# Optimization experiments

Hardware: AMD Instinct MI355X
Metric: run time of the kernel (lower is better)

## Reference

```python
import jax, jax.numpy as jnp
import numpy as np

NEG_SLOPE = 0.2
EPS = 1e-16  # PyG softmax denominator epsilon


def gatv2_layer(x, src, dst, W_l, W_r, att, bias, num_nodes, heads, out_dim, concat):
    # x: [N, F_in]; src/dst: [E] (self-loops already included)
    x_l = (x @ W_l).reshape(num_nodes, heads, out_dim)  # source transform
    x_r = (x @ W_r).reshape(num_nodes, heads, out_dim)  # target transform
    # GATv2 scoring: a^T LeakyReLU(x_l[j] + x_r[i])
    e = jax.nn.leaky_relu(x_l[src] + x_r[dst], NEG_SLOPE)       # [E, H, D]
    logits = jnp.einsum('ehd,hd->eh', e, att)                    # [E, H]
    # segment softmax over incoming edges of each target node
    m = jax.ops.segment_max(logits, dst, num_segments=num_nodes)  # [N, H]
    ex = jnp.exp(logits - m[dst])                                 # [E, H]
    denom = jax.ops.segment_sum(ex, dst, num_segments=num_nodes)  # [N, H]
    alpha = ex / (denom[dst] + EPS)                               # [E, H]
    msg = x_l[src] * alpha[:, :, None]                            # [E, H, D]
    out = jax.ops.segment_sum(msg, dst, num_segments=num_nodes)   # [N, H, D]
    if concat:
        out = out.reshape(num_nodes, heads * out_dim)
    else:
        out = out.mean(axis=1)
    return out + bias


def setup_inputs() -> dict:
    key = jax.random.key(0)
    ks = jax.random.split(key, 10)
    N, E, F_in, H, D, F_out = 50000, 400000, 256, 4, 128, 64

    def glorot(k, shape, fan):
        return jax.random.normal(k, shape, dtype=jnp.float32) * (1.0 / np.sqrt(fan))

    return {
        'x': jax.random.normal(ks[0], (N, F_in), dtype=jnp.float32),
        'edge_index': jax.random.randint(ks[1], (2, E), 0, N, dtype=jnp.int64),
        'W_l1': glorot(ks[2], (F_in, H * D), F_in),
        'W_r1': glorot(ks[3], (F_in, H * D), F_in),
        'att1': glorot(ks[4], (H, D), D),
        'b1': jnp.zeros((H * D,), dtype=jnp.float32),
        'W_l2': glorot(ks[5], (H * D, F_out), H * D),
        'W_r2': glorot(ks[6], (H * D, F_out), H * D),
        'att2': glorot(ks[7], (1, F_out), F_out),
        'b2': jnp.zeros((F_out,), dtype=jnp.float32),
    }


def reference(x, edge_index, W_l1, W_r1, att1, b1, W_l2, W_r2, att2, b2):
    N = x.shape[0]
    # add self-loops (PyG GATv2Conv default add_self_loops=True)
    loops = jnp.arange(N, dtype=edge_index.dtype)
    src = jnp.concatenate([edge_index[0], loops])
    dst = jnp.concatenate([edge_index[1], loops])
    # dropout(p=0.6) is identity in eval mode
    h = gatv2_layer(x, src, dst, W_l1, W_r1, att1, b1, N, heads=4, out_dim=128, concat=True)
    h = jax.nn.elu(h)
    out = gatv2_layer(h, src, dst, W_l2, W_r2, att2, b2, N, heads=1, out_dim=64, concat=False)
    return out
```

## Files before the change

### kernel.cpp

```cpp
#include <hip/hip_runtime.h>
#include <hip/hip_bf16.h>
#include <math.h>


#define NEG_SLOPE 0.2f
#define LOG2E 1.4426950408889634f

typedef _Float16 half8 __attribute__((ext_vector_type(8)));
typedef _Float16 h2 __attribute__((ext_vector_type(2)));
typedef float f32x4 __attribute__((ext_vector_type(4)));

#if __has_builtin(__builtin_amdgcn_global_load_lds)
#define HAS_GLL 1
__device__ __forceinline__ void gll16(const _Float16* g, _Float16* l) {
    __builtin_amdgcn_global_load_lds(
        (const __attribute__((address_space(1))) unsigned int*)g,
        (__attribute__((address_space(3))) unsigned int*)l, 16, 0, 0);
}
#endif

__device__ __forceinline__ float dot2acc(h2 a, h2 b, float c) {
#if __has_builtin(__builtin_amdgcn_fdot2)
    return __builtin_amdgcn_fdot2(a, b, c, false);
#else
    return fmaf((float)a[1], (float)b[1], fmaf((float)a[0], (float)b[0], c));
#endif
}

__device__ __forceinline__ float fast_exp2(float p) {
#if __has_builtin(__builtin_amdgcn_exp2f)
    return __builtin_amdgcn_exp2f(p);
#else
    return exp2f(p);
#endif
}


__global__ __launch_bounds__(256) void k_castx_count(const float* __restrict__ x, _Float16* __restrict__ xh,
                                                     int n8, const int* __restrict__ ei,
                                                     int* __restrict__ counts, int E, int Etot, int gEtot) {
    int b = blockIdx.x;
    if (b < gEtot) {
        int i = b * 256 + threadIdx.x;
        if (i < Etot) {
            int dst = (i < E) ? ei[E + i] : (i - E);
            atomicAdd(&counts[dst], 1);
        }
    } else {
        int i = (b - gEtot) * 256 + threadIdx.x;
        if (i < n8) {
            const float4* p = (const float4*)(x + i * 8);
            float4 a = p[0], c = p[1];
            half8 v;
            v[0] = (_Float16)a.x; v[1] = (_Float16)a.y; v[2] = (_Float16)a.z; v[3] = (_Float16)a.w;
            v[4] = (_Float16)c.x; v[5] = (_Float16)c.y; v[6] = (_Float16)c.z; v[7] = (_Float16)c.w;
            *(half8*)(xh + i * 8) = v;
        }
    }
}


__global__ __launch_bounds__(1024) void k_castw_scana(const int* __restrict__ counts, int* __restrict__ offs,
                                                      int* __restrict__ partial, int n, int nsb,
                                                      const float* __restrict__ Wl1, const float* __restrict__ Wr1,
                                                      const float* __restrict__ Wl2, const float* __restrict__ Wr2,
                                                      _Float16* __restrict__ W1T, _Float16* __restrict__ W2T) {
    __shared__ int buf[1024];
    int b = blockIdx.x, t = threadIdx.x;
    if (b < nsb) {
        int i = b * 1024 + t;
        int v = (i < n) ? counts[i] : 0;
        buf[t] = v;
        __syncthreads();
        #pragma unroll
        for (int off = 1; off < 1024; off <<= 1) {
            int add = (t >= off) ? buf[t - off] : 0;
            __syncthreads();
            buf[t] += add;
            __syncthreads();
        }
        if (i < n) offs[i + 1] = buf[t];
        if (t == 1023) partial[b] = buf[1023];
    } else {
        int i = (b - nsb) * 1024 + t;
        const int T1 = 1024 * 256;
        const int T2 = 128 * 512;
        if (i < T1) {
            int nn = i >> 8, k = i & 255;
            float v = (nn < 512) ? Wl1[k * 512 + nn] : Wr1[k * 512 + (nn - 512)];
            W1T[i] = (_Float16)v;
        } else if (i < T1 + T2) {
            int j = i - T1;
            int nn = j >> 9, k = j & 511;
            float v = (nn < 64) ? Wl2[k * 64 + nn] : Wr2[k * 64 + (nn - 64)];
            W2T[j] = (_Float16)v;
        }
    }
}


__global__ __launch_bounds__(256) void k_scanbc(int* __restrict__ offs, int* __restrict__ cursor,
                                                const int* __restrict__ partial, int n, int nsb) {
    __shared__ int s[256];
    int t = threadIdx.x;
    int v = (t < nsb) ? partial[t] : 0;
    s[t] = v;
    __syncthreads();
    #pragma unroll
    for (int off = 1; off < 256; off <<= 1) {
        int add = (t >= off) ? s[t - off] : 0;
        __syncthreads();
        s[t] += add;
        __syncthreads();
    }
    int excl = s[t] - v;
    s[t] = excl;
    __syncthreads();
    int i = blockIdx.x * 256 + t;
    if (i == 0) { offs[0] = 0; cursor[0] = 0; }
    if (i < n) {
        int w = offs[i + 1] + s[i >> 10];
        offs[i + 1] = w;
        cursor[i + 1] = w;
    }
}


__device__ __forceinline__ void gemm_body(const _Float16* __restrict__ A,
                                          const _Float16* __restrict__ Bt,
                                          _Float16* __restrict__ C,
                                          int M, int N, int K, int ntiles, int blk,
                                          _Float16* As, _Float16* Bs) {
    int tid = threadIdx.x;
    int lane = tid & 63;
    int wave = tid >> 6;
    int wm = wave >> 1, wn = wave & 1;
    int l15 = lane & 15, q = lane >> 4;

    int ntile = blk % ntiles;
    int mtile = blk / ntiles;
    int tileM = mtile * 128;
    int tileN = ntile * 128;

    int srow = lane >> 2;
    int schunk = (lane & 3) ^ ((lane >> 3) & 3);
    const _Float16* gA0 = A + (long)(tileM + wave * 32 + srow) * K + schunk * 8;
    const _Float16* gA1 = gA0 + (long)16 * K;
    const _Float16* gB0 = Bt + (long)(tileN + wave * 32 + srow) * K + schunk * 8;
    const _Float16* gB1 = gB0 + (long)16 * K;
    _Float16* lA0 = As + wave * 1024;
    _Float16* lA1 = lA0 + 512;
    _Float16* lB0 = Bs + wave * 1024;
    _Float16* lB1 = lB0 + 512;

    int aswz = (q ^ ((l15 >> 1) & 3)) * 8;

    f32x4 acc[4][4];
    #pragma unroll
    for (int i = 0; i < 4; ++i)
        #pragma unroll
        for (int j = 0; j < 4; ++j)
            acc[i][j] = (f32x4)(0.f);

    for (int k0 = 0; k0 < K; k0 += 32) {
#ifdef HAS_GLL
        gll16(gA0 + k0, lA0);
        gll16(gA1 + k0, lA1);
        gll16(gB0 + k0, lB0);
        gll16(gB1 + k0, lB1);
#else
        half8 va0 = *(const half8*)(gA0 + k0);
        half8 va1 = *(const half8*)(gA1 + k0);
        half8 vb0 = *(const half8*)(gB0 + k0);
        half8 vb1 = *(const half8*)(gB1 + k0);
        *(half8*)(lA0 + lane * 8) = va0;
        *(half8*)(lA1 + lane * 8) = va1;
        *(half8*)(lB0 + lane * 8) = vb0;
        *(half8*)(lB1 + lane * 8) = vb1;
#endif
        __syncthreads();

        half8 af[4], bf[4];
        #pragma unroll
        for (int i = 0; i < 4; ++i)
            af[i] = *(const half8*)(As + (wm * 64 + i * 16 + l15) * 32 + aswz);
        #pragma unroll
        for (int j = 0; j < 4; ++j)
            bf[j] = *(const half8*)(Bs + (wn * 64 + j * 16 + l15) * 32 + aswz);
        #pragma unroll
        for (int i = 0; i < 4; ++i)
            #pragma unroll
            for (int j = 0; j < 4; ++j)
                acc[i][j] = __builtin_amdgcn_mfma_f32_16x16x32_f16(af[i], bf[j], acc[i][j], 0, 0, 0);
        __syncthreads();
    }

    #pragma unroll
    for (int i = 0; i < 4; ++i) {
        #pragma unroll
        for (int r = 0; r < 4; ++r) {
            int grow = tileM + wm * 64 + i * 16 + q * 4 + r;
            if (grow < M) {
                #pragma unroll
                for (int j = 0; j < 4; ++j) {
                    int gcol = tileN + wn * 64 + j * 16 + l15;
                    C[(long)grow * N + gcol] = (_Float16)acc[i][j][r];
                }
            }
        }
    }
}

__global__ __launch_bounds__(256) void k_gemm1_fill(const _Float16* __restrict__ A,
                                                    const _Float16* __restrict__ Bt,
                                                    _Float16* __restrict__ C,
                                                    int M, int N, int K, int ntiles, int gb,
                                                    const int* __restrict__ ei, int* __restrict__ cursor,
                                                    int* __restrict__ csr_src, int E, int Etot) {
    __shared__ _Float16 As[128 * 32];
    __shared__ _Float16 Bs[128 * 32];
    int b = blockIdx.x;
    if (b < gb) {
        gemm_body(A, Bt, C, M, N, K, ntiles, b, As, Bs);
    } else {
        int i = (b - gb) * 256 + threadIdx.x;
        if (i < Etot) {
            int src, dst;
            if (i < E) { src = ei[i]; dst = ei[E + i]; }
            else       { src = i - E; dst = i - E; }
            int pos = atomicAdd(&cursor[dst], 1);
            csr_src[pos] = src;
        }
    }
}

__global__ __launch_bounds__(256) void k_gemm_f16(const _Float16* __restrict__ A,
                                                  const _Float16* __restrict__ Bt,
                                                  _Float16* __restrict__ C,
                                                  int M, int N, int K, int ntiles) {
    __shared__ _Float16 As[128 * 32];
    __shared__ _Float16 Bs[128 * 32];
    gemm_body(A, Bt, C, M, N, K, ntiles, blockIdx.x, As, Bs);
}


__global__ __launch_bounds__(256) void k_attn1(const _Float16* __restrict__ xlr,
                                               const float* __restrict__ att, const float* __restrict__ b1,
                                               const int* __restrict__ offs, const int* __restrict__ csr_src,
                                               _Float16* __restrict__ hout, int N) {
    int wave = threadIdx.x >> 6;
    int lane = threadIdx.x & 63;
    int node = blockIdx.x * 4 + wave;
    if (node >= N) return;

    int cbase = (lane >> 4) * 128 + (lane & 15) * 8;

    half8 xrv8 = *(const half8*)(xlr + (long)node * 1024 + 512 + cbase);
    float4 atv0 = *(const float4*)(att + cbase);
    float4 atv1 = *(const float4*)(att + cbase + 4);
    h2 xr[4], at[4];
    #pragma unroll
    for (int j = 0; j < 4; ++j) {
        xr[j][0] = xrv8[2 * j]; xr[j][1] = xrv8[2 * j + 1];
    }
    at[0][0] = (_Float16)(atv0.x * LOG2E); at[0][1] = (_Float16)(atv0.y * LOG2E);
    at[1][0] = (_Float16)(atv0.z * LOG2E); at[1][1] = (_Float16)(atv0.w * LOG2E);
    at[2][0] = (_Float16)(atv1.x * LOG2E); at[2][1] = (_Float16)(atv1.y * LOG2E);
    at[3][0] = (_Float16)(atv1.z * LOG2E); at[3][1] = (_Float16)(atv1.w * LOG2E);
    const h2 ns2 = {(_Float16)NEG_SLOPE, (_Float16)NEG_SLOPE};

    float l = 0.f;
    float acc[8] = {};

    int e0 = offs[node], e1 = offs[node + 1];
    int s_next = csr_src[e0];
    int s_next2 = (e0 + 1 < e1) ? csr_src[e0 + 1] : 0;
    half8 xlv = *(const half8*)(xlr + (long)s_next * 1024 + cbase);

    for (int e = e0; e < e1; ++e) {
        half8 cur = xlv;
        int s_pf = s_next2;
        if (e + 2 < e1) s_next2 = csr_src[e + 2];
        if (e + 1 < e1) xlv = *(const half8*)(xlr + (long)s_pf * 1024 + cbase);

        const h2* cp = (const h2*)&cur;
        float p = 0.f;
        #pragma unroll
        for (int j = 0; j < 4; ++j) {
            h2 t = cp[j] + xr[j];
#if __has_builtin(__builtin_elementwise_max)
            t = __builtin_elementwise_max(t, t * ns2);
#else
            h2 tn = t * ns2;
            t[0] = (t[0] > tn[0]) ? t[0] : tn[0];
            t[1] = (t[1] > tn[1]) ? t[1] : tn[1];
#endif
            p = dot2acc(t, at[j], p);
        }
        #pragma unroll
        for (int off = 1; off <= 8; off <<= 1) p += __shfl_xor(p, off, 64);
        float w = fast_exp2(p);
        l += w;
        #pragma unroll
        for (int j = 0; j < 8; ++j) acc[j] = fmaf(w, (float)cur[j], acc[j]);
    }

    float inv = 1.f / (l + 1e-16f);
    float4 b1v0 = *(const float4*)(b1 + cbase);
    float4 b1v1 = *(const float4*)(b1 + cbase + 4);
    float bb[8] = {b1v0.x, b1v0.y, b1v0.z, b1v0.w, b1v1.x, b1v1.y, b1v1.z, b1v1.w};
    half8 ov;
    #pragma unroll
    for (int j = 0; j < 8; ++j) {
        float o = fmaf(acc[j], inv, bb[j]);
        o = (o > 0.f) ? o : (__expf(o) - 1.f);
        ov[j] = (_Float16)o;
    }
    *(half8*)(hout + (long)node * 512 + cbase) = ov;
}


__global__ __launch_bounds__(256) void k_attn2(const _Float16* __restrict__ xlr2,
                                               const float* __restrict__ att, const float* __restrict__ b2,
                                               const int* __restrict__ offs, const int* __restrict__ csr_src,
                                               float* __restrict__ out, int N) {
    int wave = threadIdx.x >> 6;
    int lane = threadIdx.x & 63;
    int node = blockIdx.x * 4 + wave;
    if (node >= N) return;

    int eh = lane >> 5;
    int hl = lane & 31;
    int ch = hl * 2;

    h2 xrh = *(const h2*)(xlr2 + (long)node * 128 + 64 + ch);
    float2 atf = *(const float2*)(att + ch);
    h2 ath; ath[0] = (_Float16)(atf.x * LOG2E); ath[1] = (_Float16)(atf.y * LOG2E);
    const h2 ns2 = {(_Float16)NEG_SLOPE, (_Float16)NEG_SLOPE};

    float l = 0.f, a0 = 0.f, a1 = 0.f;
    int e0 = offs[node], e1 = offs[node + 1];
    int e = e0 + eh;
    h2 cv;
    if (e < e1) {
        int s = csr_src[e];
        cv = *(const h2*)(xlr2 + (long)s * 128 + ch);
    }
    while (e < e1) {
        h2 u = cv;
        int en = e + 2;
        if (en < e1) {
            int s = csr_src[en];
            cv = *(const h2*)(xlr2 + (long)s * 128 + ch);
        }
        h2 t = u + xrh;
#if __has_builtin(__builtin_elementwise_max)
        t = __builtin_elementwise_max(t, t * ns2);
#else
        h2 tn = t * ns2;
        t[0] = (t[0] > tn[0]) ? t[0] : tn[0];
        t[1] = (t[1] > tn[1]) ? t[1] : tn[1];
#endif
        float p = dot2acc(t, ath, 0.f);
        p += __shfl_xor(p, 1, 64);
        p += __shfl_xor(p, 2, 64);
        p += __shfl_xor(p, 4, 64);
        p += __shfl_xor(p, 8, 64);
        p += __shfl_xor(p, 16, 64);
        float w = fast_exp2(p);
        l += w;
        a0 = fmaf(w, (float)u[0], a0);
        a1 = fmaf(w, (float)u[1], a1);
        e = en;
    }
    l += __shfl_xor(l, 32, 64);
    a0 += __shfl_xor(a0, 32, 64);
    a1 += __shfl_xor(a1, 32, 64);
    if (eh == 0) {
        float inv = 1.f / (l + 1e-16f);
        float2 o;
        o.x = fmaf(a0, inv, b2[ch]);
        o.y = fmaf(a1, inv, b2[ch + 1]);
        *(float2*)(out + (long)node * 64 + ch) = o;
    }
}


extern "C" void kernel_launch(void* const* d_in, const int* in_sizes, int n_in,
                              void* d_out, int out_size, void* d_ws, size_t ws_size,
                              hipStream_t stream) {
    const float* x    = (const float*)d_in[0];
    const int*   ei   = (const int*)d_in[1];
    const float* Wl1  = (const float*)d_in[2];
    const float* Wr1  = (const float*)d_in[3];
    const float* att1 = (const float*)d_in[4];
    const float* b1   = (const float*)d_in[5];
    const float* Wl2  = (const float*)d_in[6];
    const float* Wr2  = (const float*)d_in[7];
    const float* att2 = (const float*)d_in[8];
    const float* b2   = (const float*)d_in[9];
    float* out = (float*)d_out;

    const int F_IN = 256;
    int N = in_sizes[0] / F_IN;
    int E = in_sizes[1] / 2;
    int Etot = E + N;
    int nScanBlocks = (N + 1023) / 1024;
    int mtiles = (N + 127) / 128;
    int Mpad = mtiles * 128;

    char* p = (char*)d_ws;
    auto carve = [&](size_t bytes) -> void* {
        void* r = (void*)p;
        p += (bytes + 255) & ~(size_t)255;
        return r;
    };
    _Float16* xh   = (_Float16*)carve((size_t)Mpad * 256 * 2);
    _Float16* W1T  = (_Float16*)carve((size_t)1024 * 256 * 2);
    _Float16* W2T  = (_Float16*)carve((size_t)128 * 512 * 2);
    _Float16* C1   = (_Float16*)carve((size_t)N * 1024 * 2);
    _Float16* h    = (_Float16*)carve((size_t)Mpad * 512 * 2);
    _Float16* C2   = (_Float16*)carve((size_t)N * 128 * 2);
    int* counts  = (int*)carve((size_t)N * 4);
    int* offs    = (int*)carve((size_t)(N + 1) * 4);
    int* cursor  = (int*)carve((size_t)(N + 1) * 4);
    int* partial = (int*)carve((size_t)nScanBlocks * 4);
    int* csr     = (int*)carve((size_t)Etot * 4);

    int gN    = (N + 255) / 256;
    int gEtot = (Etot + 255) / 256;
    int n8    = N * 256 / 8;
    int gCast = (n8 + 255) / 256;

    hipMemsetAsync(counts, 0, (size_t)N * 4, stream);

    k_castx_count<<<gEtot + gCast, 256, 0, stream>>>(x, xh, n8, ei, counts, E, Etot, gEtot);

    {
        int total = 1024 * 256 + 128 * 512;
        int gW = (total + 1023) / 1024;
        k_castw_scana<<<nScanBlocks + gW, 1024, 0, stream>>>(counts, offs, partial, N, nScanBlocks,
                                                             Wl1, Wr1, Wl2, Wr2, W1T, W2T);
    }
    k_scanbc<<<gN, 256, 0, stream>>>(offs, cursor, partial, N, nScanBlocks);

    {
        int gb = mtiles * 8;
        k_gemm1_fill<<<gb + gEtot, 256, 0, stream>>>(xh, W1T, C1, N, 1024, 256, 8, gb,
                                                     ei, cursor, csr, E, Etot);
    }
    k_attn1<<<(N + 3) / 4, 256, 0, stream>>>(C1, att1, b1, offs, csr, h, N);

    k_gemm_f16<<<mtiles, 256, 0, stream>>>(h, W2T, C2, N, 128, 512, 1);
    k_attn2<<<(N + 3) / 4, 256, 0, stream>>>(C2, att2, b2, offs, csr, out, N);
}
```

Measured before the change: 334.1 us.

## Use 512-thread GEMM blocks with 4x2 wave grid and packed FMA in attention

The GEMM kernels move from 256 to 512 threads per 128x128 tile, arranged as a 2x4 wave grid. Each wave now loads one 16-row slice per k-step and computes a 64x32 sub-tile, which cuts accumulator registers per thread and doubles the waves available to hide latency. The attention kernels switch to unsigned shift-based gather addressing and float2 vector FMAs so the compiler can emit packed FMA. The fill path is resized to 512 threads per block to match. The trade-off is less B-fragment reuse per wave and more sync participants per tile.

```diff
diff --git a/kernel.cpp b/kernel.cpp
--- a/kernel.cpp
+++ b/kernel.cpp
@@ -9,6 +9,7 @@
 typedef _Float16 half8 __attribute__((ext_vector_type(8)));
 typedef _Float16 h2 __attribute__((ext_vector_type(2)));
 typedef float f32x4 __attribute__((ext_vector_type(4)));
+typedef float f32x2 __attribute__((ext_vector_type(2)));
 
 #if __has_builtin(__builtin_amdgcn_global_load_lds)
 #define HAS_GLL 1
@@ -134,7 +135,7 @@
     int tid = threadIdx.x;
     int lane = tid & 63;
     int wave = tid >> 6;
-    int wm = wave >> 1, wn = wave & 1;
+    int wm = wave >> 2, wn = wave & 3;
     int l15 = lane & 15, q = lane >> 4;
 
     int ntile = blk % ntiles;
@@ -144,53 +145,43 @@
 
     int srow = lane >> 2;
     int schunk = (lane & 3) ^ ((lane >> 3) & 3);
-    const _Float16* gA0 = A + (long)(tileM + wave * 32 + srow) * K + schunk * 8;
-    const _Float16* gA1 = gA0 + (long)16 * K;
-    const _Float16* gB0 = Bt + (long)(tileN + wave * 32 + srow) * K + schunk * 8;
-    const _Float16* gB1 = gB0 + (long)16 * K;
-    _Float16* lA0 = As + wave * 1024;
-    _Float16* lA1 = lA0 + 512;
-    _Float16* lB0 = Bs + wave * 1024;
-    _Float16* lB1 = lB0 + 512;
+    const _Float16* gA = A + (long)(tileM + wave * 16 + srow) * K + schunk * 8;
+    const _Float16* gB = Bt + (long)(tileN + wave * 16 + srow) * K + schunk * 8;
+    _Float16* lA = As + wave * 512;
+    _Float16* lB = Bs + wave * 512;
 
     int aswz = (q ^ ((l15 >> 1) & 3)) * 8;
 
-    f32x4 acc[4][4];
+    f32x4 acc[4][2];
     #pragma unroll
     for (int i = 0; i < 4; ++i)
         #pragma unroll
-        for (int j = 0; j < 4; ++j)
+        for (int j = 0; j < 2; ++j)
             acc[i][j] = (f32x4)(0.f);
 
     for (int k0 = 0; k0 < K; k0 += 32) {
 #ifdef HAS_GLL
-        gll16(gA0 + k0, lA0);
-        gll16(gA1 + k0, lA1);
-        gll16(gB0 + k0, lB0);
-        gll16(gB1 + k0, lB1);
+        gll16(gA + k0, lA);
+        gll16(gB + k0, lB);
 #else
-        half8 va0 = *(const half8*)(gA0 + k0);
-        half8 va1 = *(const half8*)(gA1 + k0);
-        half8 vb0 = *(const half8*)(gB0 + k0);
-        half8 vb1 = *(const half8*)(gB1 + k0);
-        *(half8*)(lA0 + lane * 8) = va0;
-        *(half8*)(lA1 + lane * 8) = va1;
-        *(half8*)(lB0 + lane * 8) = vb0;
-        *(half8*)(lB1 + lane * 8) = vb1;
+        half8 va = *(const half8*)(gA + k0);
+        half8 vb = *(const half8*)(gB + k0);
+        *(half8*)(lA + lane * 8) = va;
+        *(half8*)(lB + lane * 8) = vb;
 #endif
         __syncthreads();
 
-        half8 af[4], bf[4];
+        half8 af[4], bf[2];
         #pragma unroll
         for (int i = 0; i < 4; ++i)
             af[i] = *(const half8*)(As + (wm * 64 + i * 16 + l15) * 32 + aswz);
         #pragma unroll
-        for (int j = 0; j < 4; ++j)
-            bf[j] = *(const half8*)(Bs + (wn * 64 + j * 16 + l15) * 32 + aswz);
+        for (int j = 0; j < 2; ++j)
+            bf[j] = *(const half8*)(Bs + (wn * 32 + j * 16 + l15) * 32 + aswz);
         #pragma unroll
         for (int i = 0; i < 4; ++i)
             #pragma unroll
-            for (int j = 0; j < 4; ++j)
+            for (int j = 0; j < 2; ++j)
                 acc[i][j] = __builtin_amdgcn_mfma_f32_16x16x32_f16(af[i], bf[j], acc[i][j], 0, 0, 0);
         __syncthreads();
     }
@@ -202,8 +193,8 @@
             int grow = tileM + wm * 64 + i * 16 + q * 4 + r;
             if (grow < M) {
                 #pragma unroll
-                for (int j = 0; j < 4; ++j) {
-                    int gcol = tileN + wn * 64 + j * 16 + l15;
+                for (int j = 0; j < 2; ++j) {
+                    int gcol = tileN + wn * 32 + j * 16 + l15;
                     C[(long)grow * N + gcol] = (_Float16)acc[i][j][r];
                 }
             }
@@ -211,7 +202,7 @@
     }
 }
 
-__global__ __launch_bounds__(256) void k_gemm1_fill(const _Float16* __restrict__ A,
+__global__ __launch_bounds__(512) void k_gemm1_fill(const _Float16* __restrict__ A,
                                                     const _Float16* __restrict__ Bt,
                                                     _Float16* __restrict__ C,
                                                     int M, int N, int K, int ntiles, int gb,
@@ -223,7 +214,7 @@
     if (b < gb) {
         gemm_body(A, Bt, C, M, N, K, ntiles, b, As, Bs);
     } else {
-        int i = (b - gb) * 256 + threadIdx.x;
+        int i = (b - gb) * 512 + threadIdx.x;
         if (i < Etot) {
             int src, dst;
             if (i < E) { src = ei[i]; dst = ei[E + i]; }
@@ -234,7 +225,7 @@
     }
 }
 
-__global__ __launch_bounds__(256) void k_gemm_f16(const _Float16* __restrict__ A,
+__global__ __launch_bounds__(512) void k_gemm_f16(const _Float16* __restrict__ A,
                                                   const _Float16* __restrict__ Bt,
                                                   _Float16* __restrict__ C,
                                                   int M, int N, int K, int ntiles) {
@@ -254,8 +245,9 @@
     if (node >= N) return;
 
     int cbase = (lane >> 4) * 128 + (lane & 15) * 8;
-
-    half8 xrv8 = *(const half8*)(xlr + (long)node * 1024 + 512 + cbase);
+    const _Float16* xlr_l = xlr + cbase;
+
+    half8 xrv8 = *(const half8*)(xlr_l + ((unsigned)node << 10) + 512);
     float4 atv0 = *(const float4*)(att + cbase);
     float4 atv1 = *(const float4*)(att + cbase + 4);
     h2 xr[4], at[4];
@@ -270,18 +262,20 @@
     const h2 ns2 = {(_Float16)NEG_SLOPE, (_Float16)NEG_SLOPE};
 
     float l = 0.f;
-    float acc[8] = {};
+    f32x2 acc[4];
+    #pragma unroll
+    for (int j = 0; j < 4; ++j) acc[j] = (f32x2)(0.f);
 
     int e0 = offs[node], e1 = offs[node + 1];
     int s_next = csr_src[e0];
     int s_next2 = (e0 + 1 < e1) ? csr_src[e0 + 1] : 0;
-    half8 xlv = *(const half8*)(xlr + (long)s_next * 1024 + cbase);
+    half8 xlv = *(const half8*)(xlr_l + ((unsigned)s_next << 10));
 
     for (int e = e0; e < e1; ++e) {
         half8 cur = xlv;
         int s_pf = s_next2;
         if (e + 2 < e1) s_next2 = csr_src[e + 2];
-        if (e + 1 < e1) xlv = *(const half8*)(xlr + (long)s_pf * 1024 + cbase);
+        if (e + 1 < e1) xlv = *(const half8*)(xlr_l + ((unsigned)s_pf << 10));
 
         const h2* cp = (const h2*)&cur;
         float p = 0.f;
@@ -301,8 +295,12 @@
         for (int off = 1; off <= 8; off <<= 1) p += __shfl_xor(p, off, 64);
         float w = fast_exp2(p);
         l += w;
-        #pragma unroll
-        for (int j = 0; j < 8; ++j) acc[j] = fmaf(w, (float)cur[j], acc[j]);
+        f32x2 w2 = {w, w};
+        #pragma unroll
+        for (int j = 0; j < 4; ++j) {
+            f32x2 xf = {(float)cur[2 * j], (float)cur[2 * j + 1]};
+            acc[j] = w2 * xf + acc[j];
+        }
     }
 
     float inv = 1.f / (l + 1e-16f);
@@ -312,7 +310,7 @@
     half8 ov;
     #pragma unroll
     for (int j = 0; j < 8; ++j) {
-        float o = fmaf(acc[j], inv, bb[j]);
+        float o = fmaf(acc[j >> 1][j & 1], inv, bb[j]);
         o = (o > 0.f) ? o : (__expf(o) - 1.f);
         ov[j] = (_Float16)o;
     }
@@ -332,26 +330,28 @@
     int eh = lane >> 5;
     int hl = lane & 31;
     int ch = hl * 2;
-
-    h2 xrh = *(const h2*)(xlr2 + (long)node * 128 + 64 + ch);
+    const _Float16* xlr_l = xlr2 + ch;
+
+    h2 xrh = *(const h2*)(xlr_l + ((unsigned)node << 7) + 64);
     float2 atf = *(const float2*)(att + ch);
     h2 ath; ath[0] = (_Float16)(atf.x * LOG2E); ath[1] = (_Float16)(atf.y * LOG2E);
     const h2 ns2 = {(_Float16)NEG_SLOPE, (_Float16)NEG_SLOPE};
 
-    float l = 0.f, a0 = 0.f, a1 = 0.f;
+    float l = 0.f;
+    f32x2 acc = (f32x2)(0.f);
     int e0 = offs[node], e1 = offs[node + 1];
     int e = e0 + eh;
     h2 cv;
     if (e < e1) {
         int s = csr_src[e];
-        cv = *(const h2*)(xlr2 + (long)s * 128 + ch);
+        cv = *(const h2*)(xlr_l + ((unsigned)s << 7));
     }
     while (e < e1) {
         h2 u = cv;
         int en = e + 2;
         if (en < e1) {
             int s = csr_src[en];
-            cv = *(const h2*)(xlr2 + (long)s * 128 + ch);
+            cv = *(const h2*)(xlr_l + ((unsigned)s << 7));
         }
         h2 t = u + xrh;
 #if __has_builtin(__builtin_elementwise_max)
@@ -369,18 +369,19 @@
         p += __shfl_xor(p, 16, 64);
         float w = fast_exp2(p);
         l += w;
-        a0 = fmaf(w, (float)u[0], a0);
-        a1 = fmaf(w, (float)u[1], a1);
+        f32x2 w2 = {w, w};
+        f32x2 xf = {(float)u[0], (float)u[1]};
+        acc = w2 * xf + acc;
         e = en;
     }
     l += __shfl_xor(l, 32, 64);
-    a0 += __shfl_xor(a0, 32, 64);
-    a1 += __shfl_xor(a1, 32, 64);
+    acc[0] += __shfl_xor(acc[0], 32, 64);
+    acc[1] += __shfl_xor(acc[1], 32, 64);
     if (eh == 0) {
         float inv = 1.f / (l + 1e-16f);
         float2 o;
-        o.x = fmaf(a0, inv, b2[ch]);
-        o.y = fmaf(a1, inv, b2[ch + 1]);
+        o.x = fmaf(acc[0], inv, b2[ch]);
+        o.y = fmaf(acc[1], inv, b2[ch + 1]);
         *(float2*)(out + (long)node * 64 + ch) = o;
     }
 }
@@ -446,11 +447,12 @@
 
     {
         int gb = mtiles * 8;
-        k_gemm1_fill<<<gb + gEtot, 256, 0, stream>>>(xh, W1T, C1, N, 1024, 256, 8, gb,
-                                                     ei, cursor, csr, E, Etot);
+        int fillBlocks = (Etot + 511) / 512;
+        k_gemm1_fill<<<gb + fillBlocks, 512, 0, stream>>>(xh, W1T, C1, N, 1024, 256, 8, gb,
+                                                          ei, cursor, csr, E, Etot);
     }
     k_attn1<<<(N + 3) / 4, 256, 0, stream>>>(C1, att1, b1, offs, csr, h, N);
 
-    k_gemm_f16<<<mtiles, 256, 0, stream>>>(h, W2T, C2, N, 128, 512, 1);
+    k_gemm_f16<<<mtiles, 512, 0, stream>>>(h, W2T, C2, N, 128, 512, 1);
     k_attn2<<<(N + 3) / 4, 256, 0, stream>>>(C2, att2, b2, offs, csr, out, N);
 }
```

After: 324.9 us. 2.7% less time.
